# Kernel tuning notes

Hardware: AMD Instinct MI355X
Metric: run time of the kernel (lower is better)

Reference implementation:

```python
import jax, jax.numpy as jnp
import numpy as np

B, D, H, O = 4096, 1024, 8192, 1000

def setup_inputs() -> dict:
    key = jax.random.key(0)
    k1, k2, k3 = jax.random.split(key, 3)
    x = jax.random.normal(k1, (B, D), dtype=jnp.float32)
    kohonen_weights = jax.random.normal(k2, (H, D), dtype=jnp.float32) * (6.0 / (H + D)) ** 0.5
    grossberg_weights = jax.random.normal(k3, (O, H), dtype=jnp.float32) * (6.0 / (O + H)) ** 0.5
    return {"x": x, "kohonen_weights": kohonen_weights, "grossberg_weights": grossberg_weights}

def reference(x, kohonen_weights, grossberg_weights):
    # but kept faithful since distances only feed argmin -> same winners either way)
    x_sq = jnp.sum(x * x, axis=1, keepdims=True)                      # [B,1]
    w_sq = jnp.sum(kohonen_weights * kohonen_weights, axis=1)         # [H]
    sq_dists = x_sq - 2.0 * (x @ kohonen_weights.T) + w_sq[None, :]   # [B,H]
    winners = jnp.argmin(sq_dists, axis=1)                            # [B]
    # one_hot @ grossberg.T is mathematically a row gather of grossberg.T
    output = grossberg_weights.T[winners]                             # [B,O]
    return output, winners
```

## Files before the change

kernel.cpp:

```cpp
#include <hip/hip_runtime.h>
#include <hip/hip_bf16.h>

#define B_ 4096
#define D_ 1024
#define H_ 8192
#define O_ 1000
#define K2 2048
#define NT 48
#define NITER (NT / 2)

typedef __attribute__((ext_vector_type(8))) short short8;
typedef __attribute__((ext_vector_type(4))) short short4v;
typedef __attribute__((ext_vector_type(4))) float f32x4;

union BF4 { __hip_bfloat16 b[4]; short4v s; };

__device__ __forceinline__ void gload16(void* ldsp, const void* g) {
  __builtin_amdgcn_global_load_lds(
      (const __attribute__((address_space(1))) unsigned int*)g,
      (__attribute__((address_space(3))) unsigned int*)ldsp, 16, 0, 0);
}

__device__ __forceinline__ int aoff_(int T) {
  const int t = T / 3, r = T - 3 * t;
  return (r == 1 ? 1024 : 0) + t * 64;
}
__device__ __forceinline__ int boff_(int T) {
  const int t = T / 3, r = T - 3 * t;
  return (r == 2 ? 1024 : 0) + t * 64;
}

__global__ __launch_bounds__(256) void split_all_kernel(
    const float* __restrict__ x, const float* __restrict__ w,
    __hip_bfloat16* __restrict__ Ap, __hip_bfloat16* __restrict__ Bp,
    float* __restrict__ xsq, float* __restrict__ wsq,
    unsigned long long* __restrict__ keys)
{
  const int r = blockIdx.x;
  const int t = threadIdx.x;
  const float* src;
  __hip_bfloat16* dst;
  float* sq;
  if (r < B_) {
    src = x + (size_t)r * D_; dst = Ap + (size_t)r * K2; sq = xsq + r;
    if (t == 0) keys[r] = ~0ULL;
  } else {
    const int rr = r - B_;
    src = w + (size_t)rr * D_; dst = Bp + (size_t)rr * K2; sq = wsq + rr;
  }
  const float4 v = ((const float4*)src)[t];
  float ss = v.x * v.x + v.y * v.y + v.z * v.z + v.w * v.w;

  BF4 Hh, Ll;
  const float e[4] = {v.x, v.y, v.z, v.w};
#pragma unroll
  for (int i = 0; i < 4; ++i) {
    __hip_bfloat16 h = __float2bfloat16(e[i]);
    Hh.b[i] = h;
    Ll.b[i] = __float2bfloat16(e[i] - __bfloat162float(h));
  }
  *(short4v*)(dst + t * 4) = Hh.s;
  *(short4v*)(dst + 1024 + t * 4) = Ll.s;

#pragma unroll
  for (int o = 32; o > 0; o >>= 1) ss += __shfl_down(ss, o);
  __shared__ float wsum[4];
  if ((t & 63) == 0) wsum[t >> 6] = ss;
  __syncthreads();
  if (t == 0) *sq = (wsum[0] + wsum[1]) + (wsum[2] + wsum[3]);
}


#define BAR() do { asm volatile("" ::: "memory"); \
                   __builtin_amdgcn_s_barrier(); \
                   asm volatile("" ::: "memory"); } while (0)
#define GATE8() asm volatile("s_waitcnt vmcnt(8)" ::: "memory")

#define STAGE(P, prow, T, isB, h) do { if ((T) < NT) { \
    const int koff_ = (isB) ? boff_(T) : aoff_(T); \
    const __hip_bfloat16* s_ = (P) + (size_t)((prow) + (h)*128 + wid*16 + srow) * K2 + koff_ + sunit * 8; \
    char* d_ = lds + ((T)&1)*65536 + (isB)*32768 + (h)*16384 + wid*2048 + lane*16; \
    gload16(d_, s_); gload16(d_ + 1024, s_ + 8*K2); } } while (0)

#define READ_A(dst, db, mh) do { \
    const char* p_ = lds + (db) + (mh)*16384 + (wm*64 + cc)*128; \
    _Pragma("unroll") for (int m_ = 0; m_ < 4; ++m_) { \
      dst[2*m_]   = *(const short8*)(p_ + m_*2048 + kof0); \
      dst[2*m_+1] = *(const short8*)(p_ + m_*2048 + kof1); } } while (0)

#define READ_B(dst, db, nh) do { \
    const char* p_ = lds + (db) + 32768 + (nh)*16384 + (wn*32 + cc)*128; \
    _Pragma("unroll") for (int n_ = 0; n_ < 2; ++n_) { \
      dst[2*n_]   = *(const short8*)(p_ + n_*2048 + kof0); \
      dst[2*n_+1] = *(const short8*)(p_ + n_*2048 + kof1); } } while (0)

#define MM(mh, nh, AF, BF) do { \
    __builtin_amdgcn_s_setprio(1); \
    _Pragma("unroll") for (int m_ = 0; m_ < 4; ++m_) \
    _Pragma("unroll") for (int n_ = 0; n_ < 2; ++n_) \
    _Pragma("unroll") for (int kk = 0; kk < 2; ++kk) \
      acc[(mh)*4+m_][(nh)*2+n_] = __builtin_amdgcn_mfma_f32_16x16x32_bf16( \
          AF[2*m_+kk], BF[2*n_+kk], acc[(mh)*4+m_][(nh)*2+n_], 0, 0, 0); \
    __builtin_amdgcn_s_setprio(0); } while (0)

__global__ __launch_bounds__(512, 2) void gemm_argmin_kernel(
    const __hip_bfloat16* __restrict__ Ap, const __hip_bfloat16* __restrict__ Bp,
    const float* __restrict__ xsq, const float* __restrict__ wsq,
    unsigned long long* __restrict__ keys)
{
  __shared__ char lds[131072];

  const int t = threadIdx.x;
  const int id = blockIdx.x;
  const int xcd = id & 7;
  const int r_ = id >> 3;
  const int by = (xcd >> 2) * 8 + (r_ >> 3);
  const int bx = (xcd & 3) * 8 + (r_ & 7);
  const int brow = by * 256, bcol = bx * 256;

  const int lane = t & 63, wid = t >> 6;
  const int wm = wid >> 2, wn = wid & 3;
  const int cc = lane & 15, q = lane >> 4, sw = lane & 7;
  const int kof0 = (q ^ sw) * 16;
  const int kof1 = ((4 + q) ^ sw) * 16;

  const int srow = lane >> 3;
  const int sunit = (lane & 7) ^ srow;

  f32x4 acc[8][4] = {};
  short8 aF0[8], aF1[8], bF0[4], bF1[4];

  STAGE(Ap, brow, 0, 0, 0);
  STAGE(Bp, bcol, 0, 1, 0);
  STAGE(Bp, bcol, 0, 1, 1);
  STAGE(Ap, brow, 0, 0, 1);
  STAGE(Ap, brow, 1, 0, 0);
  STAGE(Bp, bcol, 1, 1, 0);
  STAGE(Bp, bcol, 1, 1, 1);
  GATE8();
  BAR();
  READ_A(aF0, 0, 0);
  READ_B(bF0, 0, 0);

  for (int it = 0; it < NITER; ++it) {
    const int a = 2 * it, b = a + 1;
    READ_B(bF1, 0, 1);
    STAGE(Ap, brow, b, 0, 1);
    MM(0, 0, aF0, bF0);
    GATE8(); BAR();
    READ_A(aF1, 0, 1);
    STAGE(Ap, brow, a + 2, 0, 0);
    MM(0, 1, aF0, bF1);
    BAR();
    STAGE(Bp, bcol, a + 2, 1, 0);
    MM(1, 0, aF1, bF0);
    GATE8(); BAR();
    READ_A(aF0, 65536, 0);
    READ_B(bF0, 65536, 0);
    STAGE(Bp, bcol, a + 2, 1, 1);
    MM(1, 1, aF1, bF1);
    GATE8(); BAR();
    READ_B(bF1, 65536, 1);
    STAGE(Ap, brow, a + 2, 0, 1);
    MM(0, 0, aF0, bF0);
    GATE8(); BAR();
    READ_A(aF1, 65536, 1);
    STAGE(Ap, brow, b + 2, 0, 0);
    MM(0, 1, aF0, bF1);
    BAR();
    STAGE(Bp, bcol, b + 2, 1, 0);
    MM(1, 0, aF1, bF0);
    GATE8(); BAR();
    if (it + 1 < NITER) {
      READ_A(aF0, 0, 0);
      READ_B(bF0, 0, 0);
    }
    STAGE(Bp, bcol, b + 2, 1, 1);
    MM(1, 1, aF1, bF1);
    GATE8(); BAR();
  }

#pragma unroll
  for (int i = 0; i < 8; ++i) {
    const int mh = i >> 2, m_ = i & 3;
#pragma unroll
    for (int r = 0; r < 4; ++r) {
      const int row = brow + mh * 128 + wm * 64 + m_ * 16 + q * 4 + r;
      const float xs = xsq[row];
      unsigned long long best = ~0ULL;
#pragma unroll
      for (int j = 0; j < 4; ++j) {
        const int nh = j >> 1, n_ = j & 1;
        const int col = bcol + nh * 128 + wn * 32 + n_ * 16 + cc;
        const float s = (xs - 2.0f * acc[i][j][r]) + wsq[col];
        unsigned ub = __float_as_uint(s);
        ub = (ub & 0x80000000u) ? ~ub : (ub | 0x80000000u);
        const unsigned long long key =
            ((unsigned long long)ub << 32) | (unsigned)col;
        if (key < best) best = key;
      }
#pragma unroll
      for (int o = 1; o < 16; o <<= 1) {
        const unsigned long long v = __shfl_xor(best, o);
        if (v < best) best = v;
      }
      if (cc == 0) atomicMin(&keys[row], best);
    }
  }
}

__global__ __launch_bounds__(256) void transposeG_kernel(
    const float* __restrict__ G, float* __restrict__ GT)
{
  __shared__ float tile[32][33];
  const int h0 = blockIdx.x * 32;
  const int o0 = blockIdx.y * 32;
  const int tx = threadIdx.x;
  const int ty = threadIdx.y;
#pragma unroll
  for (int j = 0; j < 4; ++j) {
    const int o = o0 + ty + j * 8;
    if (o < O_) tile[ty + j * 8][tx] = G[(size_t)o * H_ + h0 + tx];
  }
  __syncthreads();
  const int o = o0 + tx;
  if (o < O_) {
#pragma unroll
    for (int j = 0; j < 4; ++j)
      GT[(size_t)(h0 + ty + j * 8) * O_ + o] = tile[tx][ty + j * 8];
  }
}

__global__ __launch_bounds__(256) void finalize_kernel(
    const unsigned long long* __restrict__ keys,
    const float* __restrict__ GT, float* __restrict__ out)
{
  const int b = blockIdx.x;
  const unsigned w = (unsigned)(keys[b] & 0xFFFFFFFFull);
  if (threadIdx.x == 0) out[(size_t)B_ * O_ + b] = (float)w;
  const float4* src = (const float4*)(GT + (size_t)w * O_);
  float4* dst = (float4*)(out + (size_t)b * O_);
  for (int i = threadIdx.x; i < O_ / 4; i += 256) dst[i] = src[i];
}

extern "C" void kernel_launch(void* const* d_in, const int* in_sizes, int n_in,
                              void* d_out, int out_size, void* d_ws, size_t ws_size,
                              hipStream_t stream)
{
  (void)in_sizes; (void)n_in; (void)out_size; (void)ws_size;
  const float* x = (const float*)d_in[0];
  const float* kw = (const float*)d_in[1];
  const float* gw = (const float*)d_in[2];
  float* out = (float*)d_out;

  char* ws = (char*)d_ws;
  __hip_bfloat16* Ap = (__hip_bfloat16*)(ws);
  __hip_bfloat16* Bp = (__hip_bfloat16*)(ws + 16777216);
  float* xsq = (float*)(ws + 50331648);
  float* wsq = (float*)(ws + 50331648 + 16384);
  unsigned long long* keys = (unsigned long long*)(ws + 50331648 + 16384 + 32768);
  float* GT = (float*)(ws);

  split_all_kernel<<<B_ + H_, 256, 0, stream>>>(x, kw, Ap, Bp, xsq, wsq, keys);
  gemm_argmin_kernel<<<512, 512, 0, stream>>>(Ap, Bp, xsq, wsq, keys);
  transposeG_kernel<<<dim3(H_ / 32, (O_ + 31) / 32), dim3(32, 8), 0, stream>>>(gw, GT);
  finalize_kernel<<<B_, 256, 0, stream>>>(keys, GT, out);
}
```

Baseline: 280.8 us.

## Reschedule GEMM main loop with single A fragment buffer and extra barriers

Rewrites the software-pipelined main loop so it keeps one A-fragment register set instead of two, reordering the quadrant MFMAs (00,01,11,10) so each A load is reused across both B halves. LDS reads, global-to-LDS stages and MFMA blocks are now split by extra barriers, and vmcnt waits are retuned, including a tail drain on the last iteration. The aim is to cut VGPR pressure, which could allow higher occupancy or less spilling. The cost is more s_barrier calls and less overlap between LDS reads and MFMA work.

```diff
diff --git a/kernel.cpp b/kernel.cpp
--- a/kernel.cpp
+++ b/kernel.cpp
@@ -74,7 +74,7 @@
 #define BAR() do { asm volatile("" ::: "memory"); \
                    __builtin_amdgcn_s_barrier(); \
                    asm volatile("" ::: "memory"); } while (0)
-#define GATE8() asm volatile("s_waitcnt vmcnt(8)" ::: "memory")
+#define GATEN(n) asm volatile("s_waitcnt vmcnt(" #n ")" ::: "memory")
 
 #define STAGE(P, prow, T, isB, h) do { if ((T) < NT) { \
     const int koff_ = (isB) ? boff_(T) : aoff_(T); \
@@ -128,7 +128,7 @@
   const int sunit = (lane & 7) ^ srow;
 
   f32x4 acc[8][4] = {};
-  short8 aF0[8], aF1[8], bF0[4], bF1[4];
+  short8 aF[8], bF0[4], bF1[4];
 
   STAGE(Ap, brow, 0, 0, 0);
   STAGE(Bp, bcol, 0, 1, 0);
@@ -137,47 +137,56 @@
   STAGE(Ap, brow, 1, 0, 0);
   STAGE(Bp, bcol, 1, 1, 0);
   STAGE(Bp, bcol, 1, 1, 1);
-  GATE8();
+  GATEN(10);
   BAR();
-  READ_A(aF0, 0, 0);
-  READ_B(bF0, 0, 0);
 
   for (int it = 0; it < NITER; ++it) {
     const int a = 2 * it, b = a + 1;
+    const bool lastit = (it == NITER - 1);
+    READ_A(aF, 0, 0);
+    READ_B(bF0, 0, 0);
+    STAGE(Ap, brow, b, 0, 1);
+    BAR();
+    MM(0, 0, aF, bF0);
+    GATEN(8);
+    BAR();
     READ_B(bF1, 0, 1);
-    STAGE(Ap, brow, b, 0, 1);
-    MM(0, 0, aF0, bF0);
-    GATE8(); BAR();
-    READ_A(aF1, 0, 1);
     STAGE(Ap, brow, a + 2, 0, 0);
-    MM(0, 1, aF0, bF1);
-    BAR();
+    BAR();
+    MM(0, 1, aF, bF1);
+    BAR();
+    READ_A(aF, 0, 1);
     STAGE(Bp, bcol, a + 2, 1, 0);
-    MM(1, 0, aF1, bF0);
-    GATE8(); BAR();
-    READ_A(aF0, 65536, 0);
+    BAR();
+    MM(1, 1, aF, bF1);
+    BAR();
+    STAGE(Bp, bcol, a + 2, 1, 1);
+    BAR();
+    MM(1, 0, aF, bF0);
+    if (lastit) { GATEN(4); } else { GATEN(10); }
+    BAR();
+    READ_A(aF, 65536, 0);
     READ_B(bF0, 65536, 0);
-    STAGE(Bp, bcol, a + 2, 1, 1);
-    MM(1, 1, aF1, bF1);
-    GATE8(); BAR();
+    STAGE(Ap, brow, a + 2, 0, 1);
+    BAR();
+    MM(0, 0, aF, bF0);
+    if (lastit) { GATEN(0); } else { GATEN(8); }
+    BAR();
     READ_B(bF1, 65536, 1);
-    STAGE(Ap, brow, a + 2, 0, 1);
-    MM(0, 0, aF0, bF0);
-    GATE8(); BAR();
-    READ_A(aF1, 65536, 1);
     STAGE(Ap, brow, b + 2, 0, 0);
-    MM(0, 1, aF0, bF1);
-    BAR();
+    BAR();
+    MM(0, 1, aF, bF1);
+    BAR();
+    READ_A(aF, 65536, 1);
     STAGE(Bp, bcol, b + 2, 1, 0);
-    MM(1, 0, aF1, bF0);
-    GATE8(); BAR();
-    if (it + 1 < NITER) {
-      READ_A(aF0, 0, 0);
-      READ_B(bF0, 0, 0);
-    }
+    BAR();
+    MM(1, 1, aF, bF1);
+    BAR();
     STAGE(Bp, bcol, b + 2, 1, 1);
-    MM(1, 1, aF1, bF1);
-    GATE8(); BAR();
+    BAR();
+    MM(1, 0, aF, bF0);
+    GATEN(10);
+    BAR();
   }
 
 #pragma unroll
```

Result: faster. 243.5 us (-13.3%).

## Rework GEMM main loop with inline-asm LDS reads and explicit waitcnt scheduling

Applied to the files above, without the earlier changes.

Replaces the compiler-scheduled LDS fragment reads with inline ds_read_b128 using precomputed base addresses, and restructures the main loop into four sub-steps per K tile with explicit lgkmcnt waits and sched_barriers. Each sub-step now covers one k-half across all four n fragments rather than both k-halves for half the n fragments. The prologue and vmcnt gates change to match a new global-load staging order. The aim is tighter overlap of LDS reads, global loads and MFMA issue with fewer barriers. The cost is that pipeline correctness now depends on hand-counted wait values.

```diff
diff --git a/kernel.cpp b/kernel.cpp
--- a/kernel.cpp
+++ b/kernel.cpp
@@ -74,7 +74,20 @@
 #define BAR() do { asm volatile("" ::: "memory"); \
                    __builtin_amdgcn_s_barrier(); \
                    asm volatile("" ::: "memory"); } while (0)
-#define GATE8() asm volatile("s_waitcnt vmcnt(8)" ::: "memory")
+#define SB0() __builtin_amdgcn_sched_barrier(0)
+#define GATE_S(S) asm volatile("s_waitcnt vmcnt(" S ")")
+#define LGKM8() do { asm volatile("s_waitcnt lgkmcnt(8)"); SB0(); } while (0)
+#define LGKM0() do { asm volatile("s_waitcnt lgkmcnt(0)"); SB0(); } while (0)
+
+#define DSR(dst, base, OFF) \
+  asm volatile("ds_read_b128 %0, %1 offset:" OFF : "=v"(dst) : "v"(base))
+
+#define RD4A(arr, base) do { unsigned _ba = (base); \
+  DSR(arr[0], _ba, "0");    DSR(arr[1], _ba, "2048"); \
+  DSR(arr[2], _ba, "4096"); DSR(arr[3], _ba, "6144"); } while (0)
+#define RD4B(arr, base) do { unsigned _bb = (base); \
+  DSR(arr[0], _bb, "0");     DSR(arr[1], _bb, "2048"); \
+  DSR(arr[2], _bb, "16384"); DSR(arr[3], _bb, "18432"); } while (0)
 
 #define STAGE(P, prow, T, isB, h) do { if ((T) < NT) { \
     const int koff_ = (isB) ? boff_(T) : aoff_(T); \
@@ -82,26 +95,45 @@
     char* d_ = lds + ((T)&1)*65536 + (isB)*32768 + (h)*16384 + wid*2048 + lane*16; \
     gload16(d_, s_); gload16(d_ + 1024, s_ + 8*K2); } } while (0)
 
-#define READ_A(dst, db, mh) do { \
-    const char* p_ = lds + (db) + (mh)*16384 + (wm*64 + cc)*128; \
-    _Pragma("unroll") for (int m_ = 0; m_ < 4; ++m_) { \
-      dst[2*m_]   = *(const short8*)(p_ + m_*2048 + kof0); \
-      dst[2*m_+1] = *(const short8*)(p_ + m_*2048 + kof1); } } while (0)
-
-#define READ_B(dst, db, nh) do { \
-    const char* p_ = lds + (db) + 32768 + (nh)*16384 + (wn*32 + cc)*128; \
-    _Pragma("unroll") for (int n_ = 0; n_ < 2; ++n_) { \
-      dst[2*n_]   = *(const short8*)(p_ + n_*2048 + kof0); \
-      dst[2*n_+1] = *(const short8*)(p_ + n_*2048 + kof1); } } while (0)
-
-#define MM(mh, nh, AF, BF) do { \
+#define MMQ(mh, A, B) do { \
     __builtin_amdgcn_s_setprio(1); \
     _Pragma("unroll") for (int m_ = 0; m_ < 4; ++m_) \
-    _Pragma("unroll") for (int n_ = 0; n_ < 2; ++n_) \
-    _Pragma("unroll") for (int kk = 0; kk < 2; ++kk) \
-      acc[(mh)*4+m_][(nh)*2+n_] = __builtin_amdgcn_mfma_f32_16x16x32_bf16( \
-          AF[2*m_+kk], BF[2*n_+kk], acc[(mh)*4+m_][(nh)*2+n_], 0, 0, 0); \
-    __builtin_amdgcn_s_setprio(0); } while (0)
+    _Pragma("unroll") for (int n_ = 0; n_ < 4; ++n_) \
+      acc[(mh)*4+m_][n_] = __builtin_amdgcn_mfma_f32_16x16x32_bf16( \
+          A[m_], B[n_], acc[(mh)*4+m_][n_], 0, 0, 0); \
+    __builtin_amdgcn_s_setprio(0); \
+    SB0(); } while (0)
+
+#define TILE4(DS, TT, G1, RDN) do { \
+     \
+    RD4A(s1A, aB01 + (DS)); \
+    RD4B(s1B, bB1  + (DS)); \
+    STAGE(Bp, bcol, (TT) + 1, 1, 1); \
+    LGKM8(); \
+    MMQ(0, s0A, s0B); \
+     \
+    GATE_S(G1); BAR(); \
+    RD4A(s0A, aB10 + (DS)); \
+    RD4B(s0B, bB0  + (DS)); \
+    STAGE(Ap, brow, (TT) + 1, 0, 0); \
+    LGKM8(); \
+    MMQ(0, s1A, s1B); \
+     \
+    RD4A(s1A, aB11 + (DS)); \
+    RD4B(s1B, bB1  + (DS)); \
+    STAGE(Ap, brow, (TT) + 1, 0, 1); \
+    LGKM8(); \
+    MMQ(1, s0A, s0B); \
+     \
+    GATE_S("2"); BAR(); \
+    if (RDN) { \
+      RD4A(s0A, aB00 + ((DS) ^ 65536)); \
+      RD4B(s0B, bB0  + ((DS) ^ 65536)); \
+      LGKM8(); \
+    } else { LGKM0(); } \
+    STAGE(Bp, bcol, (TT) + 2, 1, 0); \
+    MMQ(1, s1A, s1B); \
+  } while (0)
 
 __global__ __launch_bounds__(512, 2) void gemm_argmin_kernel(
     const __hip_bfloat16* __restrict__ Ap, const __hip_bfloat16* __restrict__ Bp,
@@ -127,57 +159,39 @@
   const int srow = lane >> 3;
   const int sunit = (lane & 7) ^ srow;
 
+  const unsigned lb = (unsigned)(uintptr_t)lds;
+  const unsigned aRow = (unsigned)((wm * 64 + cc) * 128);
+  const unsigned bRow = (unsigned)(32768 + (wn * 32 + cc) * 128);
+  const unsigned aB00 = lb + aRow + kof0;
+  const unsigned aB01 = lb + aRow + kof1;
+  const unsigned aB10 = lb + 16384 + aRow + kof0;
+  const unsigned aB11 = lb + 16384 + aRow + kof1;
+  const unsigned bB0 = lb + bRow + kof0;
+  const unsigned bB1 = lb + bRow + kof1;
+
   f32x4 acc[8][4] = {};
-  short8 aF0[8], aF1[8], bF0[4], bF1[4];
-
-  STAGE(Ap, brow, 0, 0, 0);
+  short8 s0A[4], s0B[4], s1A[4], s1B[4];
+
   STAGE(Bp, bcol, 0, 1, 0);
   STAGE(Bp, bcol, 0, 1, 1);
+  STAGE(Ap, brow, 0, 0, 0);
   STAGE(Ap, brow, 0, 0, 1);
-  STAGE(Ap, brow, 1, 0, 0);
   STAGE(Bp, bcol, 1, 1, 0);
-  STAGE(Bp, bcol, 1, 1, 1);
-  GATE8();
+  GATE_S("4");
   BAR();
-  READ_A(aF0, 0, 0);
-  READ_B(bF0, 0, 0);
-
-  for (int it = 0; it < NITER; ++it) {
-    const int a = 2 * it, b = a + 1;
-    READ_B(bF1, 0, 1);
-    STAGE(Ap, brow, b, 0, 1);
-    MM(0, 0, aF0, bF0);
-    GATE8(); BAR();
-    READ_A(aF1, 0, 1);
-    STAGE(Ap, brow, a + 2, 0, 0);
-    MM(0, 1, aF0, bF1);
-    BAR();
-    STAGE(Bp, bcol, a + 2, 1, 0);
-    MM(1, 0, aF1, bF0);
-    GATE8(); BAR();
-    READ_A(aF0, 65536, 0);
-    READ_B(bF0, 65536, 0);
-    STAGE(Bp, bcol, a + 2, 1, 1);
-    MM(1, 1, aF1, bF1);
-    GATE8(); BAR();
-    READ_B(bF1, 65536, 1);
-    STAGE(Ap, brow, a + 2, 0, 1);
-    MM(0, 0, aF0, bF0);
-    GATE8(); BAR();
-    READ_A(aF1, 65536, 1);
-    STAGE(Ap, brow, b + 2, 0, 0);
-    MM(0, 1, aF0, bF1);
-    BAR();
-    STAGE(Bp, bcol, b + 2, 1, 0);
-    MM(1, 0, aF1, bF0);
-    GATE8(); BAR();
-    if (it + 1 < NITER) {
-      READ_A(aF0, 0, 0);
-      READ_B(bF0, 0, 0);
-    }
-    STAGE(Bp, bcol, b + 2, 1, 1);
-    MM(1, 1, aF1, bF1);
-    GATE8(); BAR();
+  RD4A(s0A, aB00);
+  RD4B(s0B, bB0);
+  SB0();
+
+  for (int it = 0; it < NITER - 1; ++it) {
+    const int a = 2 * it;
+    TILE4(0,     a,     "4", 1);
+    TILE4(65536, a + 1, "4", 1);
+  }
+  {
+    const int a = 2 * (NITER - 1);
+    TILE4(0,     a,     "4", 1);
+    TILE4(65536, a + 1, "0", 0);
   }
 
 #pragma unroll
@@ -190,8 +204,7 @@
       unsigned long long best = ~0ULL;
 #pragma unroll
       for (int j = 0; j < 4; ++j) {
-        const int nh = j >> 1, n_ = j & 1;
-        const int col = bcol + nh * 128 + wn * 32 + n_ * 16 + cc;
+        const int col = bcol + (j >> 1) * 128 + wn * 32 + (j & 1) * 16 + cc;
         const float s = (xs - 2.0f * acc[i][j][r]) + wsq[col];
         unsigned ub = __float_as_uint(s);
         ub = (ub & 0x80000000u) ? ~ub : (ub | 0x80000000u);
```

Result: faster. 242.6 us (-13.6%).
